# Kernel optimization log

Measured on AMD Instinct MI355X. Metric: run time of the kernel, lower is better.

## Reference

```python
import jax, jax.numpy as jnp
import numpy as np

L = 2          # lags
D = 64         # latent_size
H = 128        # hidden_dim
NB = 3         # num_layers == n_blocks
B, T = 256, 1024


def setup_inputs() -> dict:
    key = jax.random.key(0)
    ks = jax.random.split(key, 20)
    sd = 0.1
    inp = {
        'x': jax.random.normal(ks[0], (B, T, D), jnp.float32),
        # f1: 3 hidden Linear(L*D=128 -> 128), all same shape so stacked, then out Linear(128 -> 64)
        'f1_hW': jax.random.normal(ks[1], (NB, H, H), jnp.float32) * sd,
        'f1_hb': jax.random.normal(ks[2], (NB, H), jnp.float32) * sd,
        'f1_oW': jax.random.normal(ks[3], (D, H), jnp.float32) * sd,
        'f1_ob': jax.random.normal(ks[4], (D,), jnp.float32) * sd,
        # flow: per block, s_net and t_net each Lin(D,H), Lin(H,H), Lin(H,D) (torch y = x@W.T + b)
        'sW0': jax.random.normal(ks[5], (NB, H, D), jnp.float32) * sd,
        'sb0': jax.random.normal(ks[6], (NB, H), jnp.float32) * sd,
        'sW1': jax.random.normal(ks[7], (NB, H, H), jnp.float32) * sd,
        'sb1': jax.random.normal(ks[8], (NB, H), jnp.float32) * sd,
        'sW2': jax.random.normal(ks[9], (NB, D, H), jnp.float32) * sd,
        'sb2': jax.random.normal(ks[10], (NB, D), jnp.float32) * sd,
        'tW0': jax.random.normal(ks[11], (NB, H, D), jnp.float32) * sd,
        'tb0': jax.random.normal(ks[12], (NB, H), jnp.float32) * sd,
        'tW1': jax.random.normal(ks[13], (NB, H, H), jnp.float32) * sd,
        'tb1': jax.random.normal(ks[14], (NB, H), jnp.float32) * sd,
        'tW2': jax.random.normal(ks[15], (NB, D, H), jnp.float32) * sd,
        'tb2': jax.random.normal(ks[16], (NB, D), jnp.float32) * sd,
    }
    return inp


def _leaky(z):
    return jnp.where(z >= 0, z, 0.2 * z)  # leap's NLayerLeakyMLP uses LeakyReLU(0.2)


def _flow(xt, sW0, sb0, sW1, sb1, sW2, sb2, tW0, tb0, tW1, tb1, tW2, tb2):
    # RealNVP-style affine coupling stack, no batch norm. xt: (N, D)
    m = (jnp.arange(D) % 2).astype(xt.dtype)  # alternating mask, flips per block
    u = xt
    logdet = jnp.zeros((xt.shape[0],), xt.dtype)
    for i in range(NB):
        mx = u * m
        s = jnp.tanh(mx @ sW0[i].T + sb0[i])
        s = jnp.tanh(s @ sW1[i].T + sb1[i])
        s = s @ sW2[i].T + sb2[i]
        t = jax.nn.relu(mx @ tW0[i].T + tb0[i])
        t = jax.nn.relu(t @ tW1[i].T + tb1[i])
        t = t @ tW2[i].T + tb2[i]
        u = mx + (1.0 - m) * (u - t) * jnp.exp(-s)
        logdet = logdet + jnp.sum(-(1.0 - m) * s, axis=1)
        m = 1.0 - m
    return u, logdet


def reference(x, f1_hW, f1_hb, f1_oW, f1_ob, sW0, sb0, sW1, sb1, sW2, sb2,
              tW0, tb0, tW1, tb1, tW2, tb2):
    Bs, Ts, Din = x.shape
    # f2 inverse flow on x[:, L:, :] flattened to (B*(T-L), D)
    xt = x[:, L:, :].reshape(-1, Din)
    x_inv, logdet = _flow(xt, sW0, sb0, sW1, sb1, sW2, sb2,
                          tW0, tb0, tW1, tb1, tW2, tb2)
    x_inv = x_inv.reshape(Bs, Ts - L, Din)
    # vectorized sliding-window MLP (replaces the per-timestep python loop)
    idx = jnp.arange(Ts - L)[:, None] + jnp.arange(L)        # (T-L, L)
    win = x[:, idx, :].reshape(Bs, Ts - L, L * Din)          # (B, T-L, L*D)
    h = win
    for i in range(NB):
        h = _leaky(h @ f1_hW[i].T + f1_hb[i])
    residuals = h @ f1_oW.T + f1_ob - x_inv                  # (B, T-L, D)
    log_abs_det_jacobian = jnp.sum(logdet.reshape(Bs, Ts - L), axis=1)  # (B,)
    return residuals, log_abs_det_jacobian
```

## Files before the change

kernel.cpp:

```cpp
#include <hip/hip_runtime.h>

#define DEV __device__ __forceinline__

typedef __attribute__((ext_vector_type(8)))  short bf16x8;
typedef __attribute__((ext_vector_type(4)))  short s16x4;
typedef __attribute__((ext_vector_type(4)))  float f32x4;
typedef __attribute__((ext_vector_type(16))) float f32x16;
typedef __attribute__((ext_vector_type(4)))  unsigned u32x4;

constexpr int Tt = 1024, TLr = 1022;
constexpr long WSW_BYTES = 557056;

#define MFMA32(a,b,c) __builtin_amdgcn_mfma_f32_32x32x16_bf16((a),(b),(c),0,0,0)

#define GLDS16(gp, lp) __builtin_amdgcn_global_load_lds( \
    (__attribute__((address_space(1))) void*)(void*)(gp), \
    (__attribute__((address_space(3))) void*)(void*)(lp), 16, 0, 0)

DEV short bf16hi(float f){
  unsigned u = __builtin_bit_cast(unsigned, f);
  u += 0x7FFFu + ((u >> 16) & 1u);
  return (short)(u >> 16);
}
DEV float bf2f(short h){
  unsigned u = ((unsigned)(unsigned short)h) << 16;
  return __builtin_bit_cast(float, u);
}
DEV void splitbf(float f, short &h, short &l){
  h = bf16hi(f);
  l = bf16hi(f - bf2f(h));
}

DEV unsigned cvtpk(float a, float b){
  unsigned r;
  asm("v_cvt_pk_bf16_f32 %0, %1, %2" : "=v"(r) : "v"(a), "v"(b));
  return r;
}
DEV void plswap(unsigned &a, unsigned &b){
  auto r = __builtin_amdgcn_permlane32_swap((int)a, (int)b, false, false);
  a = (unsigned)r[0]; b = (unsigned)r[1];
}

template<int A> DEV float actf(float x){
  if constexpr (A == 1){
    float e = __expf(2.f * x);
    return 1.f - 2.f * __builtin_amdgcn_rcpf(e + 1.f);
  } else if constexpr (A == 2){
    return fmaxf(x, 0.f);
  } else if constexpr (A == 3){
    return x >= 0.f ? x : 0.2f * x;
  }
  return x;
}

DEV void prefStage(const char* __restrict__ wsW, long k, char* dst, int tid){
  const char* s = wsW + (k << 14);
  #pragma unroll
  for (int it = 0; it < 4; ++it)
    GLDS16(s + it * 4096 + tid * 16, dst + it * 4096 + tid * 16);
}

DEV void packTile(const f32x16& c, unsigned (&Bg0)[4], unsigned (&Bg1)[4]){
  unsigned p0 = cvtpk(c[0], c[1]),  p1 = cvtpk(c[2], c[3]);
  unsigned p2 = cvtpk(c[4], c[5]),  p3 = cvtpk(c[6], c[7]);
  plswap(p0, p2); plswap(p1, p3);
  Bg0[0] = p0; Bg0[1] = p1; Bg0[2] = p2; Bg0[3] = p3;
  p0 = cvtpk(c[8],  c[9]);  p1 = cvtpk(c[10], c[11]);
  p2 = cvtpk(c[12], c[13]); p3 = cvtpk(c[14], c[15]);
  plswap(p0, p2); plswap(p1, p3);
  Bg1[0] = p0; Bg1[1] = p1; Bg1[2] = p2; Bg1[3] = p3;
}

template<int KT,int G,int GI,int MOUT,bool LO,int ACT,int MODE>
DEV void computeMT(const char* __restrict__ Ws, const float* __restrict__ bias,
                   const unsigned (&Bin)[2][8][4], unsigned (&Bout)[2][8][4],
                   f32x16 (&uA)[2][2], float (&ldet)[2],
                   float* __restrict__ residBase, int keep, int rowW,
                   int lane, int h4)
{
  constexpr int BS = LO ? 2048 : 1024;
  f32x16 acc[2];
  #pragma unroll
  for (int q = 0; q < 4; ++q){
    f32x4 bv = *(const f32x4*)(bias + 32 * MOUT + 8 * q + h4);
    #pragma unroll
    for (int j = 0; j < 4; ++j){ acc[0][4*q+j] = bv[j]; acc[1][4*q+j] = bv[j]; }
  }
  __builtin_amdgcn_s_setprio(1);
  #pragma unroll
  for (int kt = 0; kt < KT; ++kt){
    const char* wp = Ws + (kt * G + GI) * BS + lane * 16;
    bf16x8 Ah = *(const bf16x8*)wp;
    #pragma unroll
    for (int n = 0; n < 2; ++n){
      u32x4 bw = {Bin[n][kt][0], Bin[n][kt][1], Bin[n][kt][2], Bin[n][kt][3]};
      acc[n] = MFMA32(Ah, __builtin_bit_cast(bf16x8, bw), acc[n]);
    }
    if constexpr (LO){
      bf16x8 Al = *(const bf16x8*)(wp + 1024);
      #pragma unroll
      for (int n = 0; n < 2; ++n){
        u32x4 bw = {Bin[n][kt][0], Bin[n][kt][1], Bin[n][kt][2], Bin[n][kt][3]};
        acc[n] = MFMA32(Al, __builtin_bit_cast(bf16x8, bw), acc[n]);
      }
    }
  }
  __builtin_amdgcn_s_setprio(0);
  if constexpr (MODE == 0){
    #pragma unroll
    for (int n = 0; n < 2; ++n){
      #pragma unroll
      for (int i = 0; i < 16; ++i) acc[n][i] = actf<ACT>(acc[n][i]);
      packTile(acc[n], Bout[n][2 * MOUT], Bout[n][2 * MOUT + 1]);
    }
  } else if constexpr (MODE == 1){
    #pragma unroll
    for (int n = 0; n < 2; ++n)
      #pragma unroll
      for (int r = 0; r < 16; ++r)
        if ((r & 1) != keep) uA[MOUT][n][r] -= acc[n][r];
  } else if constexpr (MODE == 2){
    #pragma unroll
    for (int n = 0; n < 2; ++n)
      #pragma unroll
      for (int r = 0; r < 16; ++r)
        if ((r & 1) != keep){
          uA[MOUT][n][r] *= __expf(-acc[n][r]);
          ldet[n] -= acc[n][r];
        }
  } else {
    const int col = lane & 31;
    #pragma unroll
    for (int n = 0; n < 2; ++n){
      const int tau = rowW + n * 32 + col;
      if (tau < TLr){
        float* rp = residBase + (long)tau * 64 + 32 * MOUT + h4;
        #pragma unroll
        for (int q = 0; q < 4; ++q){
          f32x4 st;
          #pragma unroll
          for (int j = 0; j < 4; ++j)
            st[j] = acc[n][4 * q + j] - uA[MOUT][n][4 * q + j];
          *(f32x4*)(rp + 8 * q) = st;
        }
      }
    }
  }
}

DEV void buildMaskedB(const f32x16 (&u)[2][2], unsigned (&B)[2][8][4], int keep){
  const float mOdd  = (keep == 1) ? 1.f : 0.f;
  const float mEven = 1.f - mOdd;
  #pragma unroll
  for (int n = 0; n < 2; ++n)
    #pragma unroll
    for (int mi = 0; mi < 2; ++mi){
      f32x16 v;
      #pragma unroll
      for (int r = 0; r < 16; ++r)
        v[r] = u[mi][n][r] * ((r & 1) ? mOdd : mEven);
      packTile(v, B[n][2 * mi], B[n][2 * mi + 1]);
    }
}

DEV void buildWin(unsigned (&B)[2][8][4], const float* __restrict__ xb,
                  int rowW, int lane){
  const int col = lane & 31, h = lane >> 5;
  #pragma unroll
  for (int n = 0; n < 2; ++n){
    const int tau = rowW + n * 32 + col;
    #pragma unroll
    for (int g = 0; g < 8; ++g){
      int xr = tau + (g >= 4 ? 1 : 0);
      if (xr > Tt - 1) xr = Tt - 1;
      const int fo = (16 * g + 8 * h) & 63;
      const float* p = xb + xr * 64 + fo;
      f32x4 a = *(const f32x4*)p, b = *(const f32x4*)(p + 4);
      B[n][g][0] = cvtpk(a[0], a[1]); B[n][g][1] = cvtpk(a[2], a[3]);
      B[n][g][2] = cvtpk(b[0], b[1]); B[n][g][3] = cvtpk(b[2], b[3]);
    }
  }
}

__global__ void pnl_conv(const float* __restrict__ sW0, const float* __restrict__ sW1,
                         const float* __restrict__ sW2, const float* __restrict__ tW0,
                         const float* __restrict__ tW1, const float* __restrict__ tW2,
                         const float* __restrict__ f1_hW, const float* __restrict__ f1_oW,
                         char* __restrict__ wsW)
{
  const int cid = blockIdx.x * 256 + threadIdx.x;
  const float* src; long base; int hs, unit, BS, lg; bool LO;
  if (cid < 24576){
    const int blk = cid >> 13, r = cid & 8191;
    const long bb = (long)blk * 147456;
    if      (r < 1024){ src = tW0 + blk*8192;  hs=6; base=bb;        BS=1024; lg=2; LO=false; unit=r; }
    else if (r < 3072){ src = tW1 + blk*16384; hs=7; base=bb+16384;  BS=1024; lg=1; LO=false; unit=r-1024; }
    else if (r < 4096){ src = tW2 + blk*8192;  hs=7; base=bb+49152;  BS=1024; lg=1; LO=false; unit=r-3072; }
    else if (r < 5120){ src = sW0 + blk*8192;  hs=6; base=bb+65536;  BS=1024; lg=2; LO=false; unit=r-4096; }
    else if (r < 7168){ src = sW1 + blk*16384; hs=7; base=bb+81920;  BS=1024; lg=1; LO=false; unit=r-5120; }
    else              { src = sW2 + blk*8192;  hs=7; base=bb+114688; BS=2048; lg=0; LO=true;  unit=r-7168; }
  } else {
    const int r = cid - 24576;
    if (r < 6144){ const int l = r >> 11; src = f1_hW + l*16384; hs=7; base=442368+(long)l*32768; BS=1024; lg=1; LO=false; unit=r&2047; }
    else         { src = f1_oW; hs=7; base=540672; BS=1024; lg=1; LO=false; unit=r-6144; }
  }
  const int e    = unit << 3;
  const int feat = e >> hs;
  const int k    = e & ((1 << hs) - 1);
  const int m    = feat >> 5;
  const int stage = m >> lg;
  const int gi    = m & ((1 << lg) - 1);
  const int lane  = (feat & 31) | (((k >> 3) & 1) << 5);
  const long off  = base + (long)stage * 16384
                  + (long)((((k >> 4) << lg) + gi) * BS) + lane * 16;
  const float* sp = src + ((long)feat << hs) + k;
  f32x4 v0 = *(const f32x4*)sp, v1 = *(const f32x4*)(sp + 4);
  s16x4 ha, hb, la, lb;
  #pragma unroll
  for (int j = 0; j < 4; ++j){
    short hh, ll;
    splitbf(v0[j], hh, ll); ha[j] = hh; la[j] = ll;
    splitbf(v1[j], hh, ll); hb[j] = hh; lb[j] = ll;
  }
  *(s16x4*)(wsW + off)     = ha;
  *(s16x4*)(wsW + off + 8) = hb;
  if (LO){
    *(s16x4*)(wsW + off + 1024)     = la;
    *(s16x4*)(wsW + off + 1024 + 8) = lb;
  }
}

#define CMT(KT,G,GI,MOUT,LO,ACT,MODE,WS,BIAS,BIN,BOUT) \
  computeMT<KT,G,GI,MOUT,LO,ACT,MODE>(WS,BIAS,BIN,BOUT,uA,ldet,residBase,keep,rowW,lane,h4)

__global__ __launch_bounds__(256, 2)
void pnl_main(const float* __restrict__ x,
              const float* __restrict__ f1_hb, const float* __restrict__ f1_ob,
              const float* __restrict__ sb0, const float* __restrict__ sb1,
              const float* __restrict__ sb2, const float* __restrict__ tb0,
              const float* __restrict__ tb1, const float* __restrict__ tb2,
              const char* __restrict__ wsW,
              float* __restrict__ resid, float* __restrict__ wsPart)
{
  __shared__ __align__(16) char Wb[2][16384];

  const int tid  = threadIdx.x, w = tid >> 6, lane = tid & 63;
  const int col  = lane & 31, h4 = (lane >> 5) * 4;
  const int bIdx = blockIdx.x >> 2;
  const int t0w  = (blockIdx.x & 3) << 8;
  const int rowW = t0w + w * 64;
  const float* xb = x + (long)bIdx * Tt * 64;
  float* __restrict__ residBase = resid + (long)bIdx * TLr * 64;

  prefStage(wsW, 0, Wb[0], tid);

  f32x16 uA[2][2];
  #pragma unroll
  for (int mi = 0; mi < 2; ++mi)
    #pragma unroll
    for (int n = 0; n < 2; ++n){
      int xr = rowW + n * 32 + col + 2; if (xr > Tt - 1) xr = Tt - 1;
      #pragma unroll
      for (int q = 0; q < 4; ++q){
        f32x4 v = *(const f32x4*)(xb + xr * 64 + 32 * mi + 8 * q + h4);
        #pragma unroll
        for (int j = 0; j < 4; ++j) uA[mi][n][4 * q + j] = v[j];
      }
    }

  float ldet[2] = {0.f, 0.f};
  unsigned Bx[2][8][4], By[2][8][4];

  buildMaskedB(uA, Bx, 1);
  __syncthreads();

  #pragma unroll 1
  for (int blk = 0; blk < 3; ++blk){
    const int kb = blk * 9;
    const int par = kb & 1;
    char* const WA = Wb[par];
    char* const WB = Wb[par ^ 1];
    const int keep = 1 - (blk & 1);
    const float* tb0b = tb0 + blk * 128; const float* tb1b = tb1 + blk * 128;
    const float* tb2b = tb2 + blk * 64;
    const float* sb0b = sb0 + blk * 128; const float* sb1b = sb1 + blk * 128;
    const float* sb2b = sb2 + blk * 64;

    prefStage(wsW, kb + 1, WB, tid);
    CMT(4,4,0,0,false,2,0, WA, tb0b, Bx, By);
    CMT(4,4,1,1,false,2,0, WA, tb0b, Bx, By);
    CMT(4,4,2,2,false,2,0, WA, tb0b, Bx, By);
    CMT(4,4,3,3,false,2,0, WA, tb0b, Bx, By);
    __syncthreads();
    prefStage(wsW, kb + 2, WA, tid);
    CMT(8,2,0,0,false,2,0, WB, tb1b, By, Bx);
    CMT(8,2,1,1,false,2,0, WB, tb1b, By, Bx);
    __syncthreads();
    prefStage(wsW, kb + 3, WB, tid);
    CMT(8,2,0,2,false,2,0, WA, tb1b, By, Bx);
    CMT(8,2,1,3,false,2,0, WA, tb1b, By, Bx);
    __syncthreads();
    prefStage(wsW, kb + 4, WA, tid);
    CMT(8,2,0,0,false,0,1, WB, tb2b, Bx, By);
    CMT(8,2,1,1,false,0,1, WB, tb2b, Bx, By);
    buildMaskedB(uA, By, keep);
    __syncthreads();
    prefStage(wsW, kb + 5, WB, tid);
    CMT(4,4,0,0,false,1,0, WA, sb0b, By, Bx);
    CMT(4,4,1,1,false,1,0, WA, sb0b, By, Bx);
    CMT(4,4,2,2,false,1,0, WA, sb0b, By, Bx);
    CMT(4,4,3,3,false,1,0, WA, sb0b, By, Bx);
    __syncthreads();
    prefStage(wsW, kb + 6, WA, tid);
    CMT(8,2,0,0,false,1,0, WB, sb1b, Bx, By);
    CMT(8,2,1,1,false,1,0, WB, sb1b, Bx, By);
    __syncthreads();
    prefStage(wsW, kb + 7, WB, tid);
    CMT(8,2,0,2,false,1,0, WA, sb1b, Bx, By);
    CMT(8,2,1,3,false,1,0, WA, sb1b, Bx, By);
    __syncthreads();
    prefStage(wsW, kb + 8, WA, tid);
    CMT(8,1,0,0,true,0,2, WB, sb2b, By, Bx);
    __syncthreads();
    prefStage(wsW, kb + 9, WB, tid);
    CMT(8,1,0,1,true,0,2, WA, sb2b, By, Bx);
    if (blk < 2) buildMaskedB(uA, Bx, 1 - ((blk + 1) & 1));
    else         buildWin(Bx, xb, rowW, lane);
    __syncthreads();
  }

  {
    const int keep = 0;
    char* const F1 = Wb[1];
    char* const F0 = Wb[0];
    prefStage(wsW, 28, F0, tid);
    CMT(8,2,0,0,false,3,0, F1, f1_hb, Bx, By);
    CMT(8,2,1,1,false,3,0, F1, f1_hb, Bx, By);
    __syncthreads();
    prefStage(wsW, 29, F1, tid);
    CMT(8,2,0,2,false,3,0, F0, f1_hb, Bx, By);
    CMT(8,2,1,3,false,3,0, F0, f1_hb, Bx, By);
    __syncthreads();
    prefStage(wsW, 30, F0, tid);
    CMT(8,2,0,0,false,3,0, F1, f1_hb + 128, By, Bx);
    CMT(8,2,1,1,false,3,0, F1, f1_hb + 128, By, Bx);
    __syncthreads();
    prefStage(wsW, 31, F1, tid);
    CMT(8,2,0,2,false,3,0, F0, f1_hb + 128, By, Bx);
    CMT(8,2,1,3,false,3,0, F0, f1_hb + 128, By, Bx);
    __syncthreads();
    prefStage(wsW, 32, F0, tid);
    CMT(8,2,0,0,false,3,0, F1, f1_hb + 256, Bx, By);
    CMT(8,2,1,1,false,3,0, F1, f1_hb + 256, Bx, By);
    __syncthreads();
    prefStage(wsW, 33, F1, tid);
    CMT(8,2,0,2,false,3,0, F0, f1_hb + 256, Bx, By);
    CMT(8,2,1,3,false,3,0, F0, f1_hb + 256, Bx, By);
    __syncthreads();
    CMT(8,2,0,0,false,0,3, F1, f1_ob, By, Bx);
    CMT(8,2,1,1,false,0,3, F1, f1_ob, By, Bx);
  }

  const int tau0 = rowW + col, tau1 = rowW + 32 + col;
  float s = (tau0 < TLr ? ldet[0] : 0.f) + (tau1 < TLr ? ldet[1] : 0.f);
  #pragma unroll
  for (int off = 1; off < 64; off <<= 1) s += __shfl_xor(s, off);
  if (lane == 0) wsPart[blockIdx.x * 4 + w] = s;
}

__global__ void pnl_ldet(const float* __restrict__ ws, float* __restrict__ outLd){
  const int b = threadIdx.x;
  float s = 0.f;
  #pragma unroll
  for (int t = 0; t < 16; ++t) s += ws[b * 16 + t];
  outLd[b] = s;
}

extern "C" void kernel_launch(void* const* d_in, const int* in_sizes, int n_in,
                              void* d_out, int out_size, void* d_ws, size_t ws_size,
                              hipStream_t stream){
  const float* x     = (const float*)d_in[0];
  const float* f1_hW = (const float*)d_in[1];
  const float* f1_hb = (const float*)d_in[2];
  const float* f1_oW = (const float*)d_in[3];
  const float* f1_ob = (const float*)d_in[4];
  const float* sW0   = (const float*)d_in[5];
  const float* sb0   = (const float*)d_in[6];
  const float* sW1   = (const float*)d_in[7];
  const float* sb1   = (const float*)d_in[8];
  const float* sW2   = (const float*)d_in[9];
  const float* sb2   = (const float*)d_in[10];
  const float* tW0   = (const float*)d_in[11];
  const float* tb0   = (const float*)d_in[12];
  const float* tW1   = (const float*)d_in[13];
  const float* tb1   = (const float*)d_in[14];
  const float* tW2   = (const float*)d_in[15];
  const float* tb2   = (const float*)d_in[16];

  char*  wsW    = (char*)d_ws;
  float* wsPart = (float*)(wsW + WSW_BYTES);
  float* resid  = (float*)d_out;
  float* outLd  = resid + (long)256 * TLr * 64;

  pnl_conv<<<dim3(124), dim3(256), 0, stream>>>(sW0, sW1, sW2, tW0, tW1, tW2,
                                                f1_hW, f1_oW, wsW);
  pnl_main<<<dim3(1024), dim3(256), 0, stream>>>(
      x, f1_hb, f1_ob, sb0, sb1, sb2, tb0, tb1, tb2, wsW, resid, wsPart);
  pnl_ldet<<<dim3(1), dim3(256), 0, stream>>>(wsPart, outLd);
}
```

Measured before the change: 199.8 us.

## Skip masked-out input columns in first coupling layers by packing only kept features

The first layer of each s/t coupling net multiplies a masked input in which half the features are zero. The change packs only the kept (odd or even) features into the MFMA operand, halving the K dimension of those GEMMs (KT 4 to 2). The weight-conversion kernel writes a compacted, parity-specific weight layout to match. The corresponding weight stages are prefetched at half size. This removes wasted MFMA work and weight bandwidth, but adds tricky index remapping that must match the operand packing exactly.

```diff
diff --git a/kernel.cpp b/kernel.cpp
--- a/kernel.cpp
+++ b/kernel.cpp
@@ -57,6 +57,12 @@
   const char* s = wsW + (k << 14);
   #pragma unroll
   for (int it = 0; it < 4; ++it)
+    GLDS16(s + it * 4096 + tid * 16, dst + it * 4096 + tid * 16);
+}
+DEV void prefStage8(const char* __restrict__ wsW, long k, char* dst, int tid){
+  const char* s = wsW + (k << 14);
+  #pragma unroll
+  for (int it = 0; it < 2; ++it)
     GLDS16(s + it * 4096 + tid * 16, dst + it * 4096 + tid * 16);
 }
 
@@ -148,19 +154,19 @@
   }
 }
 
-DEV void buildMaskedB(const f32x16 (&u)[2][2], unsigned (&B)[2][8][4], int keep){
-  const float mOdd  = (keep == 1) ? 1.f : 0.f;
-  const float mEven = 1.f - mOdd;
+template<int KEEP>
+DEV void buildPackedMxT(const f32x16 (&u)[2][2], unsigned (&B)[2][8][4]){
   #pragma unroll
   for (int n = 0; n < 2; ++n)
     #pragma unroll
-    for (int mi = 0; mi < 2; ++mi){
-      f32x16 v;
-      #pragma unroll
-      for (int r = 0; r < 16; ++r)
-        v[r] = u[mi][n][r] * ((r & 1) ? mOdd : mEven);
-      packTile(v, B[n][2 * mi], B[n][2 * mi + 1]);
-    }
+    for (int mi = 0; mi < 2; ++mi)
+      #pragma unroll
+      for (int a = 0; a < 4; ++a)
+        B[n][mi][a] = cvtpk(u[mi][n][4*a + KEEP], u[mi][n][4*a + KEEP + 2]);
+}
+DEV void buildPackedMx(const f32x16 (&u)[2][2], unsigned (&B)[2][8][4], int keep){
+  if (keep) buildPackedMxT<1>(u, B);
+  else      buildPackedMxT<0>(u, B);
 }
 
 DEV void buildWin(unsigned (&B)[2][8][4], const float* __restrict__ xb,
@@ -190,13 +196,15 @@
 {
   const int cid = blockIdx.x * 256 + threadIdx.x;
   const float* src; long base; int hs, unit, BS, lg; bool LO;
+  bool PK = false; int keepBit = 0;
   if (cid < 24576){
     const int blk = cid >> 13, r = cid & 8191;
     const long bb = (long)blk * 147456;
-    if      (r < 1024){ src = tW0 + blk*8192;  hs=6; base=bb;        BS=1024; lg=2; LO=false; unit=r; }
+    keepBit = 1 - (blk & 1);
+    if      (r < 1024){ src = tW0 + blk*8192;  hs=6; base=bb;        BS=1024; lg=2; LO=false; unit=r; PK=true; }
     else if (r < 3072){ src = tW1 + blk*16384; hs=7; base=bb+16384;  BS=1024; lg=1; LO=false; unit=r-1024; }
     else if (r < 4096){ src = tW2 + blk*8192;  hs=7; base=bb+49152;  BS=1024; lg=1; LO=false; unit=r-3072; }
-    else if (r < 5120){ src = sW0 + blk*8192;  hs=6; base=bb+65536;  BS=1024; lg=2; LO=false; unit=r-4096; }
+    else if (r < 5120){ src = sW0 + blk*8192;  hs=6; base=bb+65536;  BS=1024; lg=2; LO=false; unit=r-4096; PK=true; }
     else if (r < 7168){ src = sW1 + blk*16384; hs=7; base=bb+81920;  BS=1024; lg=1; LO=false; unit=r-5120; }
     else              { src = sW2 + blk*8192;  hs=7; base=bb+114688; BS=2048; lg=0; LO=true;  unit=r-7168; }
   } else {
@@ -207,14 +215,31 @@
   const int e    = unit << 3;
   const int feat = e >> hs;
   const int k    = e & ((1 << hs) - 1);
+  const float* sp = src + ((long)feat << hs) + k;
+  f32x4 v0 = *(const f32x4*)sp, v1 = *(const f32x4*)(sp + 4);
+
+  if (PK){
+    #pragma unroll
+    for (int j = 0; j < 8; ++j){
+      const int c = k + j;
+      if ((c & 1) == keepBit){
+        const int kp   = 16*(c>>5) + 8*((c>>2)&1) + 2*((c>>3)&3) + ((c&3)>>1);
+        const int lane = (feat & 31) | (((kp >> 3) & 1) << 5);
+        const long off = base + (long)((((kp >> 4) << 2) + (feat >> 5)) * 1024)
+                       + lane * 16 + (kp & 7) * 2;
+        const float val = (j < 4) ? v0[j] : v1[j - 4];
+        *(short*)(wsW + off) = bf16hi(val);
+      }
+    }
+    return;
+  }
+
   const int m    = feat >> 5;
   const int stage = m >> lg;
   const int gi    = m & ((1 << lg) - 1);
   const int lane  = (feat & 31) | (((k >> 3) & 1) << 5);
   const long off  = base + (long)stage * 16384
                   + (long)((((k >> 4) << lg) + gi) * BS) + lane * 16;
-  const float* sp = src + ((long)feat << hs) + k;
-  f32x4 v0 = *(const f32x4*)sp, v1 = *(const f32x4*)(sp + 4);
   s16x4 ha, hb, la, lb;
   #pragma unroll
   for (int j = 0; j < 4; ++j){
@@ -252,7 +277,7 @@
   const float* xb = x + (long)bIdx * Tt * 64;
   float* __restrict__ residBase = resid + (long)bIdx * TLr * 64;
 
-  prefStage(wsW, 0, Wb[0], tid);
+  prefStage8(wsW, 0, Wb[0], tid);
 
   f32x16 uA[2][2];
   #pragma unroll
@@ -271,7 +296,7 @@
   float ldet[2] = {0.f, 0.f};
   unsigned Bx[2][8][4], By[2][8][4];
 
-  buildMaskedB(uA, Bx, 1);
+  buildPackedMx(uA, Bx, 1);
   __syncthreads();
 
   #pragma unroll 1
@@ -287,10 +312,10 @@
     const float* sb2b = sb2 + blk * 64;
 
     prefStage(wsW, kb + 1, WB, tid);
-    CMT(4,4,0,0,false,2,0, WA, tb0b, Bx, By);
-    CMT(4,4,1,1,false,2,0, WA, tb0b, Bx, By);
-    CMT(4,4,2,2,false,2,0, WA, tb0b, Bx, By);
-    CMT(4,4,3,3,false,2,0, WA, tb0b, Bx, By);
+    CMT(2,4,0,0,false,2,0, WA, tb0b, Bx, By);
+    CMT(2,4,1,1,false,2,0, WA, tb0b, Bx, By);
+    CMT(2,4,2,2,false,2,0, WA, tb0b, Bx, By);
+    CMT(2,4,3,3,false,2,0, WA, tb0b, Bx, By);
     __syncthreads();
     prefStage(wsW, kb + 2, WA, tid);
     CMT(8,2,0,0,false,2,0, WB, tb1b, By, Bx);
@@ -300,16 +325,16 @@
     CMT(8,2,0,2,false,2,0, WA, tb1b, By, Bx);
     CMT(8,2,1,3,false,2,0, WA, tb1b, By, Bx);
     __syncthreads();
-    prefStage(wsW, kb + 4, WA, tid);
+    prefStage8(wsW, kb + 4, WA, tid);
     CMT(8,2,0,0,false,0,1, WB, tb2b, Bx, By);
     CMT(8,2,1,1,false,0,1, WB, tb2b, Bx, By);
-    buildMaskedB(uA, By, keep);
+    buildPackedMx(uA, By, keep);
     __syncthreads();
     prefStage(wsW, kb + 5, WB, tid);
-    CMT(4,4,0,0,false,1,0, WA, sb0b, By, Bx);
-    CMT(4,4,1,1,false,1,0, WA, sb0b, By, Bx);
-    CMT(4,4,2,2,false,1,0, WA, sb0b, By, Bx);
-    CMT(4,4,3,3,false,1,0, WA, sb0b, By, Bx);
+    CMT(2,4,0,0,false,1,0, WA, sb0b, By, Bx);
+    CMT(2,4,1,1,false,1,0, WA, sb0b, By, Bx);
+    CMT(2,4,2,2,false,1,0, WA, sb0b, By, Bx);
+    CMT(2,4,3,3,false,1,0, WA, sb0b, By, Bx);
     __syncthreads();
     prefStage(wsW, kb + 6, WA, tid);
     CMT(8,2,0,0,false,1,0, WB, sb1b, Bx, By);
@@ -322,9 +347,10 @@
     prefStage(wsW, kb + 8, WA, tid);
     CMT(8,1,0,0,true,0,2, WB, sb2b, By, Bx);
     __syncthreads();
-    prefStage(wsW, kb + 9, WB, tid);
+    if (blk < 2) prefStage8(wsW, kb + 9, WB, tid);
+    else         prefStage (wsW, kb + 9, WB, tid);
     CMT(8,1,0,1,true,0,2, WA, sb2b, By, Bx);
-    if (blk < 2) buildMaskedB(uA, Bx, 1 - ((blk + 1) & 1));
+    if (blk < 2) buildPackedMx(uA, Bx, 1 - ((blk + 1) & 1));
     else         buildWin(Bx, xb, rowW, lane);
     __syncthreads();
   }
```

New measurement: 200.0 us. Within noise of the previous version (+0.1%).
